# Kernel tuning notes

Measured on AMD Instinct MI355X. Metric: run time of the kernel, lower is better.

Reference implementation:

```python
import jax, jax.numpy as jnp
import numpy as np

P = 4   # patch_size
S = 2   # patch_stride


def setup_inputs() -> dict:
    key = jax.random.key(0)
    ks = jax.random.split(key, 7)
    img    = jax.random.uniform(ks[0], (8, 1, 1024, 1024), dtype=jnp.float32)
    w_conv = jax.random.normal(ks[1], (2, 1, 2, 2), dtype=jnp.float32) * 0.5  # Conv2d(1,2,k=2,s=2)
    b_conv = jax.random.normal(ks[2], (2,), dtype=jnp.float32) * 0.1
    W_b    = jax.random.normal(ks[3], (2, 2), dtype=jnp.float32) * 0.5        # Linear(2,2)
    b_b    = jax.random.normal(ks[4], (2,), dtype=jnp.float32) * 0.1
    W_d    = jax.random.normal(ks[5], (2, 1, 2, 2), dtype=jnp.float32) * 0.5  # ConvTranspose2d(2,1,k=2,s=2)
    b_d    = jax.random.normal(ks[6], (1,), dtype=jnp.float32) * 0.1
    return dict(img=img, w_conv=w_conv, b_conv=b_conv, W_b=W_b, b_b=b_b, W_d=W_d, b_d=b_d)


def reference(img, w_conv, b_conv, W_b, b_b, W_d, b_d):
    B, _, H, Wd_ = img.shape
    nj = (H - P) // S + 1
    nk = (Wd_ - P) // S + 1

    # gather indices for patch extraction / overlap-add
    rows = (jnp.arange(nj) * S)[:, None] + jnp.arange(P)[None, :]  # (nj, P)
    cols = (jnp.arange(nk) * S)[:, None] + jnp.arange(P)[None, :]  # (nk, P)
    r = rows[:, None, :, None]  # (nj, 1, P, 1)
    c = cols[None, :, None, :]  # (1, nk, 1, P)

    # extract all overlapping patches: (B, nj, nk, P, P)
    patches = img[:, 0][:, r, c]
    N = B * nj * nk
    p = patches.reshape(N, P, P)

    # Conv2d(1->2, kernel 2, stride 2) + ReLU; non-overlapping 2x2 blocks
    blocks = p.reshape(N, 2, 2, 2, 2)                 # (N, j2, ph, k2, pw)
    conv = jnp.einsum('njpkq,cpq->ncjk', blocks, w_conv[:, 0]) + b_conv[None, :, None, None]
    conv = jax.nn.relu(conv)                          # (N, 2, 2, 2)

    # MaxPool2d(2,2) with indices (row-major within 2x2 window)
    flat = conv.reshape(N, 2, 4)
    idx = jnp.argmax(flat, axis=-1)                   # (N, 2) int
    vals = jnp.max(flat, axis=-1)                     # (N, 2)

    # bottleneck: Linear(2,2) + ReLU
    z = jax.nn.relu(vals @ W_b.T + b_b)               # (N, 2)

    # MaxUnpool2d -> (N, 2, 2, 2)
    unp = (z[..., None] * jax.nn.one_hot(idx, 4, dtype=z.dtype)).reshape(N, 2, 2, 2)

    # ConvTranspose2d(2->1, kernel 2, stride 2) + Sigmoid: out[2i+p, 2j+q]
    dec = jnp.einsum('ncij,cpq->nipjq', unp, W_d[:, 0]).reshape(N, P, P) + b_d[0]
    dec = jax.nn.sigmoid(dec).reshape(B, nj, nk, P, P)

    # overlap-add fold + count normalization
    out = jnp.zeros((B, H, Wd_), dtype=img.dtype).at[:, r, c].add(dec)
    count = jnp.zeros((H, Wd_), dtype=img.dtype).at[r, c].add(1.0)
    return (out / count)[:, None]  # (B, 1, H, W)
```

## Files before the change

### kernel.cpp

```cpp
#include <hip/hip_runtime.h>

#define IMG_H 1024
#define IMG_W 1024

static __device__ __forceinline__ int iclamp(int v, int lo, int hi) {
    return v < lo ? lo : (v > hi ? hi : v);
}

__global__ __launch_bounds__(256) void ae_fused(
    const float* __restrict__ img,
    const float* __restrict__ w_conv,
    const float* __restrict__ b_conv,
    const float* __restrict__ W_b,
    const float* __restrict__ b_b,
    const float* __restrict__ W_d,
    const float* __restrict__ b_d,
    float* __restrict__ out)
{
    const int n = blockIdx.x * blockDim.x + threadIdx.x;
    const int m = blockIdx.y;
    const int b = blockIdx.z;

    float wc[2][4], wd[2][4], wb[2][2];
    #pragma unroll
    for (int c = 0; c < 2; ++c) {
        #pragma unroll
        for (int t = 0; t < 4; ++t) {
            wc[c][t] = w_conv[c * 4 + t];
            wd[c][t] = W_d[c * 4 + t];
        }
    }
    wb[0][0] = W_b[0]; wb[0][1] = W_b[1];
    wb[1][0] = W_b[2]; wb[1][1] = W_b[3];
    const float bc0 = b_conv[0], bc1 = b_conv[1];
    const float bb0 = b_b[0],   bb1 = b_b[1];
    const float bd  = b_d[0];

    float reg[6][6];
    const float* imgb = img + (size_t)b * IMG_H * IMG_W;
    #pragma unroll
    for (int r = 0; r < 6; ++r) {
        const int gr = iclamp(2 * m - 2 + r, 0, IMG_H - 1);
        const float* rowp = imgb + (size_t)gr * IMG_W;
        #pragma unroll
        for (int cc = 0; cc < 3; ++cc) {
            const int gc = iclamp(2 * n - 2 + 2 * cc, 0, IMG_W - 2);
            const float2 v = *(const float2*)(rowp + gc);
            reg[r][2 * cc]     = v.x;
            reg[r][2 * cc + 1] = v.y;
        }
    }

    const int vr0 = (m >= 1);
    const int vr1 = (m <= 510);
    const int vc0 = (n >= 1);
    const int vc1 = (n <= 510);
    const float rcnt = 1.0f / (float)((vr0 + vr1) * (vc0 + vc1));

    float acc[2][2] = {{0.f, 0.f}, {0.f, 0.f}};

    #pragma unroll
    for (int a = 0; a < 2; ++a) {
        if (!(a ? vr1 : vr0)) continue;
        const int br = 2 * a;
        const int iq = 1 - a;
        #pragma unroll
        for (int e = 0; e < 2; ++e) {
            if (!(e ? vc1 : vc0)) continue;
            const int bc = 2 * e;
            const int jq = 1 - e;
            const int tm = iq * 2 + jq;

            float v0[4], v1[4];
            #pragma unroll
            for (int j = 0; j < 2; ++j) {
                #pragma unroll
                for (int k = 0; k < 2; ++k) {
                    const float p00 = reg[br + 2 * j][bc + 2 * k];
                    const float p01 = reg[br + 2 * j][bc + 2 * k + 1];
                    const float p10 = reg[br + 2 * j + 1][bc + 2 * k];
                    const float p11 = reg[br + 2 * j + 1][bc + 2 * k + 1];
                    float s0 = p00 * wc[0][0] + p01 * wc[0][1] + p10 * wc[0][2] + p11 * wc[0][3] + bc0;
                    float s1 = p00 * wc[1][0] + p01 * wc[1][1] + p10 * wc[1][2] + p11 * wc[1][3] + bc1;
                    v0[j * 2 + k] = fmaxf(s0, 0.0f);
                    v1[j * 2 + k] = fmaxf(s1, 0.0f);
                }
            }
            int i0 = 0, i1 = 0;
            float m0 = v0[0], m1 = v1[0];
            #pragma unroll
            for (int t = 1; t < 4; ++t) {
                if (v0[t] > m0) { m0 = v0[t]; i0 = t; }
                if (v1[t] > m1) { m1 = v1[t]; i1 = t; }
            }
            const float z0 = fmaxf(m0 * wb[0][0] + m1 * wb[0][1] + bb0, 0.0f);
            const float z1 = fmaxf(m0 * wb[1][0] + m1 * wb[1][1] + bb1, 0.0f);
            const float g0 = (i0 == tm) ? z0 : 0.0f;
            const float g1 = (i1 == tm) ? z1 : 0.0f;
            #pragma unroll
            for (int p = 0; p < 2; ++p) {
                #pragma unroll
                for (int q = 0; q < 2; ++q) {
                    const float t2 = g0 * wd[0][p * 2 + q] + g1 * wd[1][p * 2 + q] + bd;
                    acc[p][q] += 1.0f / (1.0f + __expf(-t2));
                }
            }
        }
    }

    float* outb = out + (size_t)b * IMG_H * IMG_W;
    float2 o0 = make_float2(acc[0][0] * rcnt, acc[0][1] * rcnt);
    float2 o1 = make_float2(acc[1][0] * rcnt, acc[1][1] * rcnt);
    *(float2*)(outb + (size_t)(2 * m)     * IMG_W + 2 * n) = o0;
    *(float2*)(outb + (size_t)(2 * m + 1) * IMG_W + 2 * n) = o1;
}

extern "C" void kernel_launch(void* const* d_in, const int* in_sizes, int n_in,
                              void* d_out, int out_size, void* d_ws, size_t ws_size,
                              hipStream_t stream) {
    const float* img    = (const float*)d_in[0];
    const float* w_conv = (const float*)d_in[1];
    const float* b_conv = (const float*)d_in[2];
    const float* W_b    = (const float*)d_in[3];
    const float* b_b    = (const float*)d_in[4];
    const float* W_d    = (const float*)d_in[5];
    const float* b_d    = (const float*)d_in[6];
    float* out = (float*)d_out;

    dim3 block(256, 1, 1);
    dim3 grid(512 / 256, 512, 8);
    ae_fused<<<grid, block, 0, stream>>>(img, w_conv, b_conv, W_b, b_b, W_d, b_d, out);
}
```

Before: 118.8 us.

## Compute each patch once into shared memory, then overlap-add per tile

Before this change, each thread recomputed the encoder for all four overlapping patches that cover its 2x2 output block, so every patch was evaluated about four times. Now each 16x16 tile block computes its 17x17 patches once and writes the decoded 4x4 patch values to LDS. After a barrier, each thread sums four quadrants from LDS. Decoder sigmoids are also cut: the zero-input quadrants are filled with a constant sigmoid(bd), and only the argmax quadrants get real sigmoids. The cost is LDS traffic, a __syncthreads, and a halo of 289 patches handled by 256 threads, so some threads do two.

After: 107.0 us. 10.0% less time.

```diff
diff --git a/kernel.cpp b/kernel.cpp
--- a/kernel.cpp
+++ b/kernel.cpp
@@ -2,10 +2,10 @@
 
 #define IMG_H 1024
 #define IMG_W 1024
-
-static __device__ __forceinline__ int iclamp(int v, int lo, int hi) {
-    return v < lo ? lo : (v > hi ? hi : v);
-}
+#define TILES 16
+#define NPJ 17
+#define NPATCH (NPJ * NPJ)
+#define PSTR 20
 
 __global__ __launch_bounds__(256) void ae_fused(
     const float* __restrict__ img,
@@ -17,17 +17,20 @@
     const float* __restrict__ b_d,
     float* __restrict__ out)
 {
-    const int n = blockIdx.x * blockDim.x + threadIdx.x;
-    const int m = blockIdx.y;
-    const int b = blockIdx.z;
+    __shared__ __align__(16) float dec[NPATCH * PSTR];
+
+    const int t  = threadIdx.x;
+    const int n0 = blockIdx.x * TILES;
+    const int m0 = blockIdx.y * TILES;
+    const int b  = blockIdx.z;
 
     float wc[2][4], wd[2][4], wb[2][2];
     #pragma unroll
     for (int c = 0; c < 2; ++c) {
         #pragma unroll
-        for (int t = 0; t < 4; ++t) {
-            wc[c][t] = w_conv[c * 4 + t];
-            wd[c][t] = W_d[c * 4 + t];
+        for (int q = 0; q < 4; ++q) {
+            wc[c][q] = w_conv[c * 4 + q];
+            wd[c][q] = W_d[c * 4 + q];
         }
     }
     wb[0][0] = W_b[0]; wb[0][1] = W_b[1];
@@ -36,83 +39,102 @@
     const float bb0 = b_b[0],   bb1 = b_b[1];
     const float bd  = b_d[0];
 
-    float reg[6][6];
     const float* imgb = img + (size_t)b * IMG_H * IMG_W;
-    #pragma unroll
-    for (int r = 0; r < 6; ++r) {
-        const int gr = iclamp(2 * m - 2 + r, 0, IMG_H - 1);
-        const float* rowp = imgb + (size_t)gr * IMG_W;
-        #pragma unroll
-        for (int cc = 0; cc < 3; ++cc) {
-            const int gc = iclamp(2 * n - 2 + 2 * cc, 0, IMG_W - 2);
-            const float2 v = *(const float2*)(rowp + gc);
-            reg[r][2 * cc]     = v.x;
-            reg[r][2 * cc + 1] = v.y;
-        }
-    }
-
-    const int vr0 = (m >= 1);
-    const int vr1 = (m <= 510);
-    const int vc0 = (n >= 1);
-    const int vc1 = (n <= 510);
-    const float rcnt = 1.0f / (float)((vr0 + vr1) * (vc0 + vc1));
-
-    float acc[2][2] = {{0.f, 0.f}, {0.f, 0.f}};
 
     #pragma unroll
-    for (int a = 0; a < 2; ++a) {
-        if (!(a ? vr1 : vr0)) continue;
-        const int br = 2 * a;
-        const int iq = 1 - a;
-        #pragma unroll
-        for (int e = 0; e < 2; ++e) {
-            if (!(e ? vc1 : vc0)) continue;
-            const int bc = 2 * e;
-            const int jq = 1 - e;
-            const int tm = iq * 2 + jq;
+    for (int it = 0; it < 2; ++it) {
+        const int lp = t + it * 256;
+        if (lp < NPATCH) {
+            const int lpj = lp / NPJ;
+            const int lpk = lp - lpj * NPJ;
+            const int j = m0 - 1 + lpj;
+            const int k = n0 - 1 + lpk;
+            float* d = &dec[lp * PSTR];
+            if (j >= 0 && j <= 510 && k >= 0 && k <= 510) {
+                float p[4][4];
+                const float* base = imgb + (size_t)(2 * j) * IMG_W + 2 * k;
+                #pragma unroll
+                for (int r = 0; r < 4; ++r) {
+                    const float2 va = *(const float2*)(base + (size_t)r * IMG_W);
+                    const float2 vb = *(const float2*)(base + (size_t)r * IMG_W + 2);
+                    p[r][0] = va.x; p[r][1] = va.y; p[r][2] = vb.x; p[r][3] = vb.y;
+                }
+                float v0[4], v1[4];
+                #pragma unroll
+                for (int jj = 0; jj < 2; ++jj) {
+                    #pragma unroll
+                    for (int kk = 0; kk < 2; ++kk) {
+                        const float p00 = p[2 * jj][2 * kk];
+                        const float p01 = p[2 * jj][2 * kk + 1];
+                        const float p10 = p[2 * jj + 1][2 * kk];
+                        const float p11 = p[2 * jj + 1][2 * kk + 1];
+                        const float s0 = p00 * wc[0][0] + p01 * wc[0][1] + p10 * wc[0][2] + p11 * wc[0][3] + bc0;
+                        const float s1 = p00 * wc[1][0] + p01 * wc[1][1] + p10 * wc[1][2] + p11 * wc[1][3] + bc1;
+                        v0[jj * 2 + kk] = fmaxf(s0, 0.0f);
+                        v1[jj * 2 + kk] = fmaxf(s1, 0.0f);
+                    }
+                }
+                int i0 = 0, i1 = 0;
+                float mx0 = v0[0], mx1 = v1[0];
+                #pragma unroll
+                for (int q = 1; q < 4; ++q) {
+                    if (v0[q] > mx0) { mx0 = v0[q]; i0 = q; }
+                    if (v1[q] > mx1) { mx1 = v1[q]; i1 = q; }
+                }
+                const float z0 = fmaxf(mx0 * wb[0][0] + mx1 * wb[0][1] + bb0, 0.0f);
+                const float z1 = fmaxf(mx0 * wb[1][0] + mx1 * wb[1][1] + bb1, 0.0f);
 
-            float v0[4], v1[4];
-            #pragma unroll
-            for (int j = 0; j < 2; ++j) {
+                const float sc = 1.0f / (1.0f + __expf(-bd));
+                const float4 cq = make_float4(sc, sc, sc, sc);
                 #pragma unroll
-                for (int k = 0; k < 2; ++k) {
-                    const float p00 = reg[br + 2 * j][bc + 2 * k];
-                    const float p01 = reg[br + 2 * j][bc + 2 * k + 1];
-                    const float p10 = reg[br + 2 * j + 1][bc + 2 * k];
-                    const float p11 = reg[br + 2 * j + 1][bc + 2 * k + 1];
-                    float s0 = p00 * wc[0][0] + p01 * wc[0][1] + p10 * wc[0][2] + p11 * wc[0][3] + bc0;
-                    float s1 = p00 * wc[1][0] + p01 * wc[1][1] + p10 * wc[1][2] + p11 * wc[1][3] + bc1;
-                    v0[j * 2 + k] = fmaxf(s0, 0.0f);
-                    v1[j * 2 + k] = fmaxf(s1, 0.0f);
+                for (int qd = 0; qd < 4; ++qd) *(float4*)(d + qd * 4) = cq;
+
+                {
+                    const float g0 = z0;
+                    const float g1 = (i1 == i0) ? z1 : 0.0f;
+                    float4 q;
+                    q.x = 1.0f / (1.0f + __expf(-(g0 * wd[0][0] + g1 * wd[1][0] + bd)));
+                    q.y = 1.0f / (1.0f + __expf(-(g0 * wd[0][1] + g1 * wd[1][1] + bd)));
+                    q.z = 1.0f / (1.0f + __expf(-(g0 * wd[0][2] + g1 * wd[1][2] + bd)));
+                    q.w = 1.0f / (1.0f + __expf(-(g0 * wd[0][3] + g1 * wd[1][3] + bd)));
+                    *(float4*)(d + i0 * 4) = q;
                 }
-            }
-            int i0 = 0, i1 = 0;
-            float m0 = v0[0], m1 = v1[0];
-            #pragma unroll
-            for (int t = 1; t < 4; ++t) {
-                if (v0[t] > m0) { m0 = v0[t]; i0 = t; }
-                if (v1[t] > m1) { m1 = v1[t]; i1 = t; }
-            }
-            const float z0 = fmaxf(m0 * wb[0][0] + m1 * wb[0][1] + bb0, 0.0f);
-            const float z1 = fmaxf(m0 * wb[1][0] + m1 * wb[1][1] + bb1, 0.0f);
-            const float g0 = (i0 == tm) ? z0 : 0.0f;
-            const float g1 = (i1 == tm) ? z1 : 0.0f;
-            #pragma unroll
-            for (int p = 0; p < 2; ++p) {
+                {
+                    const float g0 = (i0 == i1) ? z0 : 0.0f;
+                    const float g1 = z1;
+                    float4 q;
+                    q.x = 1.0f / (1.0f + __expf(-(g0 * wd[0][0] + g1 * wd[1][0] + bd)));
+                    q.y = 1.0f / (1.0f + __expf(-(g0 * wd[0][1] + g1 * wd[1][1] + bd)));
+                    q.z = 1.0f / (1.0f + __expf(-(g0 * wd[0][2] + g1 * wd[1][2] + bd)));
+                    q.w = 1.0f / (1.0f + __expf(-(g0 * wd[0][3] + g1 * wd[1][3] + bd)));
+                    *(float4*)(d + i1 * 4) = q;
+                }
+            } else {
+                const float4 zq = make_float4(0.0f, 0.0f, 0.0f, 0.0f);
                 #pragma unroll
-                for (int q = 0; q < 2; ++q) {
-                    const float t2 = g0 * wd[0][p * 2 + q] + g1 * wd[1][p * 2 + q] + bd;
-                    acc[p][q] += 1.0f / (1.0f + __expf(-t2));
-                }
+                for (int qd = 0; qd < 4; ++qd) *(float4*)(d + qd * 4) = zq;
             }
         }
     }
+    __syncthreads();
 
+    const int ty = t >> 4, tx = t & 15;
+    const int m = m0 + ty, n = n0 + tx;
+    float a0 = 0.f, a1 = 0.f, a2 = 0.f, a3 = 0.f;
+    #pragma unroll
+    for (int a = 0; a < 2; ++a) {
+        #pragma unroll
+        for (int e = 0; e < 2; ++e) {
+            const int lp = (ty + a) * NPJ + (tx + e);
+            const int qd = (1 - a) * 2 + (1 - e);
+            const float4 q = *(const float4*)(dec + lp * PSTR + qd * 4);
+            a0 += q.x; a1 += q.y; a2 += q.z; a3 += q.w;
+        }
+    }
+    const float rcnt = 1.0f / (float)(((m >= 1) + (m <= 510)) * ((n >= 1) + (n <= 510)));
     float* outb = out + (size_t)b * IMG_H * IMG_W;
-    float2 o0 = make_float2(acc[0][0] * rcnt, acc[0][1] * rcnt);
-    float2 o1 = make_float2(acc[1][0] * rcnt, acc[1][1] * rcnt);
-    *(float2*)(outb + (size_t)(2 * m)     * IMG_W + 2 * n) = o0;
-    *(float2*)(outb + (size_t)(2 * m + 1) * IMG_W + 2 * n) = o1;
+    *(float2*)(outb + (size_t)(2 * m) * IMG_W + 2 * n)     = make_float2(a0 * rcnt, a1 * rcnt);
+    *(float2*)(outb + (size_t)(2 * m + 1) * IMG_W + 2 * n) = make_float2(a2 * rcnt, a3 * rcnt);
 }
 
 extern "C" void kernel_launch(void* const* d_in, const int* in_sizes, int n_in,
@@ -128,6 +150,6 @@
     float* out = (float*)d_out;
 
     dim3 block(256, 1, 1);
-    dim3 grid(512 / 256, 512, 8);
+    dim3 grid(512 / TILES, 512 / TILES, 8);
     ae_fused<<<grid, block, 0, stream>>>(img, w_conv, b_conv, W_b, b_b, W_d, b_d, out);
 }
```
